# Kernel tuning notes

Measured on AMD Instinct MI355X. Metric: run time of the kernel, lower is better.

## Reference

```python
import jax, jax.numpy as jnp
import numpy as np

U, I, H, E, EL = 100000, 50000, 128, 600000, 200000


def setup_inputs() -> dict:
    key = jax.random.key(0)
    ks = jax.random.split(key, 24)
    inp = {}
    inp["user_emb"] = jax.random.normal(ks[0], (U, H), jnp.float32) * 0.1
    inp["item_emb"] = jax.random.normal(ks[1], (I, H), jnp.float32) * 0.1
    s = 1.0 / np.sqrt(H)
    names = ["w1_ui_l", "w1_ui_r", "w1_iu_l", "w1_iu_r",
             "w2_ui_l", "w2_ui_r", "w2_iu_l", "w2_iu_r"]
    for i, n in enumerate(names):
        inp[n] = jax.random.uniform(ks[2 + i], (H, H), jnp.float32, -s, s)
    for i, n in enumerate(["b1_ui", "b1_iu", "b2_ui", "b2_iu"]):
        inp[n] = jax.random.uniform(ks[10 + i], (H,), jnp.float32, -s, s)
    inp["user_node_id"] = jnp.arange(U, dtype=jnp.int32)
    inp["item_node_id"] = jnp.arange(I, dtype=jnp.int32)
    src_u = jax.random.randint(ks[14], (E,), 0, U, jnp.int32)
    dst_i = jax.random.randint(ks[15], (E,), 0, I, jnp.int32)
    inp["edge_index_ui"] = jnp.stack([src_u, dst_i])  # user -> item
    inp["edge_index_iu"] = jnp.stack([dst_i, src_u])  # item -> user (reverse)
    lu = jax.random.randint(ks[16], (EL,), 0, U, jnp.int32)
    li = jax.random.randint(ks[17], (EL,), 0, I, jnp.int32)
    inp["edge_label_index"] = jnp.stack([lu, li])
    return inp


def _sage(x_src, x_dst, edge_index, w_l, b_l, w_r, num_dst):
    # PyG SAGEConv: out = lin_l(mean_j x_src[j]) + lin_r(x_dst)
    src, dst = edge_index[0], edge_index[1]
    msg = x_src[src]                                   # [E, H] gather
    agg = jax.ops.segment_sum(msg, dst, num_segments=num_dst)
    cnt = jax.ops.segment_sum(jnp.ones((msg.shape[0],), msg.dtype), dst,
                              num_segments=num_dst)
    mean = agg / jnp.maximum(cnt, 1.0)[:, None]
    return mean @ w_l + b_l + x_dst @ w_r


def reference(user_emb, item_emb,
              w1_ui_l, w1_ui_r, w1_iu_l, w1_iu_r,
              w2_ui_l, w2_ui_r, w2_iu_l, w2_iu_r,
              b1_ui, b1_iu, b2_ui, b2_iu,
              user_node_id, item_node_id,
              edge_index_ui, edge_index_iu, edge_label_index):
    xu = user_emb[user_node_id]   # [U, H]
    xi = item_emb[item_node_id]   # [I, H]
    # layer 1 (hetero: each dst type aggregates from its single incoming relation)
    u1 = jax.nn.relu(_sage(xi, xu, edge_index_iu, w1_iu_l, b1_iu, w1_iu_r, U))
    i1 = jax.nn.relu(_sage(xu, xi, edge_index_ui, w1_ui_l, b1_ui, w1_ui_r, I))
    # layer 2
    u2 = _sage(i1, u1, edge_index_iu, w2_iu_l, b2_iu, w2_iu_r, U)
    i2 = _sage(u1, i1, edge_index_ui, w2_ui_l, b2_ui, w2_ui_r, I)
    # edge-indexed dot-product classifier
    fu = u2[edge_label_index[0]]  # [EL, H]
    fi = i2[edge_label_index[1]]  # [EL, H]
    return jnp.sum(fu * fi, axis=-1)
```

## Files before the change

### kernel.cpp

```cpp
#include <hip/hip_runtime.h>
#include <hip/hip_bf16.h>
#include <cstdio>

#define U_N 100000
#define I_N 50000
#define H_DIM 128
#define E_N 600000
#define EL_N 200000

#define EPB 2048
#define NBLK ((E_N + EPB - 1) / EPB)
#define SH_U 8
#define SH_I 7
#define NB_U ((U_N + 255) >> 8)
#define NB_I ((I_N + 127) >> 7)
#define LH_U (NB_U * NBLK)
#define LH_I (NB_I * NBLK)
#define LH_TOT (LH_U + LH_I)

#define CVT_BLK (((U_N + I_N) * 16) / 256)
#define PREP_BLK 512
#define NBU2 ((U_N + 255) / 256)
#define NBI2 ((I_N + 255) / 256)

typedef __attribute__((ext_vector_type(8))) short bh8;
typedef __attribute__((ext_vector_type(4))) float f32x4;
typedef __attribute__((ext_vector_type(8))) unsigned short u16x8;

__device__ inline unsigned short f2b(float f) {
  unsigned u = __builtin_bit_cast(unsigned, f);
  u += 0x7fffu + ((u >> 16) & 1u);
  return (unsigned short)(u >> 16);
}
__device__ inline float b2f(unsigned short h) {
  unsigned u = ((unsigned)h) << 16;
  return __builtin_bit_cast(float, u);
}

__global__ __launch_bounds__(256) void prep_all(
    const float* __restrict__ xu, const float* __restrict__ xi,
    const int* __restrict__ unid, const int* __restrict__ inid,
    unsigned short* __restrict__ ub, unsigned short* __restrict__ ib,
    const float* __restrict__ l0, const float* __restrict__ r0, short* __restrict__ o0,
    const float* __restrict__ l1, const float* __restrict__ r1, short* __restrict__ o1,
    const float* __restrict__ l2, const float* __restrict__ r2, short* __restrict__ o2,
    const float* __restrict__ l3, const float* __restrict__ r3, short* __restrict__ o3,
    const int* __restrict__ e_ui, int* __restrict__ hist) {
  __shared__ int h[512];
  const int b = blockIdx.x;
  const int tid = threadIdx.x;
  if (b < CVT_BLK) {
    int t = b * 256 + tid;
    const float* x;
    unsigned short* xb;
    int row, seg;
    if (t < U_N * 16) {
      row = t >> 4; seg = t & 15;
      int r0_ = row;
      row = unid ? unid[row] : row;
      x = xu; xb = ub + (size_t)r0_ * H_DIM;
    } else {
      int t2 = t - U_N * 16;
      row = t2 >> 4; seg = t2 & 15;
      int r0_ = row;
      row = inid ? inid[row] : row;
      x = xi; xb = ib + (size_t)r0_ * H_DIM;
    }
    const float* p = x + (size_t)row * H_DIM + seg * 8;
    float4 a = ((const float4*)p)[0];
    float4 c = ((const float4*)p)[1];
    u16x8 v;
    v[0] = f2b(a.x); v[1] = f2b(a.y); v[2] = f2b(a.z); v[3] = f2b(a.w);
    v[4] = f2b(c.x); v[5] = f2b(c.y); v[6] = f2b(c.z); v[7] = f2b(c.w);
    *(u16x8*)(xb + seg * 8) = v;
  } else if (b < CVT_BLK + PREP_BLK) {
    int t = (b - CVT_BLK) * 256 + tid;
    int set = t >> 15, s = t & 32767;
    const float *wl, *wr; short* W2;
    if (set == 0)      { wl = l0; wr = r0; W2 = o0; }
    else if (set == 1) { wl = l1; wr = r1; W2 = o1; }
    else if (set == 2) { wl = l2; wr = r2; W2 = o2; }
    else               { wl = l3; wr = r3; W2 = o3; }
    int col = s >> 8, k = s & 255;
    float v = (k < 128) ? wl[k * 128 + col] : wr[(k - 128) * 128 + col];
    W2[col * 256 + k] = (short)f2b(v);
  } else {
    int hb = b - CVT_BLK - PREP_BLK;
    int side = hb >= NBLK;
    int blk = side ? hb - NBLK : hb;
    const int* dst = e_ui + (side ? E_N : 0);
    int shift = side ? SH_I : SH_U;
    int nbins = side ? NB_I : NB_U;
    int hbase = side ? LH_U : 0;
    for (int i = tid; i < nbins; i += 256) h[i] = 0;
    __syncthreads();
    const int base = blk * EPB;
    const int end = min(base + EPB, E_N);
    for (int i = base + tid; i < end; i += 256)
      atomicAdd(&h[((unsigned)dst[i]) >> shift], 1);
    __syncthreads();
    for (int i = tid; i < nbins; i += 256)
      hist[hbase + i * NBLK + blk] = h[i];
  }
}

__global__ __launch_bounds__(256) void scan_p1(const int* __restrict__ cnt,
                                               int* __restrict__ bsum, int n) {
  const int t = threadIdx.x;
  const int base = blockIdx.x * 1024 + t * 4;
  int s = 0;
  for (int j = 0; j < 4; ++j) {
    int i = base + j;
    if (i < n) s += cnt[i];
  }
  for (int off = 32; off > 0; off >>= 1) s += __shfl_down(s, off, 64);
  __shared__ int wsum[4];
  if ((t & 63) == 0) wsum[t >> 6] = s;
  __syncthreads();
  if (t == 0) bsum[blockIdx.x] = wsum[0] + wsum[1] + wsum[2] + wsum[3];
}

__global__ __launch_bounds__(256) void scan_p2(int* __restrict__ bsum, int nb) {
  __shared__ int sm[256];
  const int t = threadIdx.x;
  int v = (t < nb) ? bsum[t] : 0;
  sm[t] = v;
  __syncthreads();
  for (int d = 1; d < 256; d <<= 1) {
    int x = (t >= d) ? sm[t - d] : 0;
    __syncthreads();
    sm[t] += x;
    __syncthreads();
  }
  if (t < nb) bsum[t] = sm[t] - v;
}

__global__ __launch_bounds__(256) void scan_p3(const int* __restrict__ cnt,
                                               const int* __restrict__ bsum,
                                               int* __restrict__ off, int n) {
  const int t = threadIdx.x;
  const int lane = t & 63, wv = t >> 6;
  const int base = blockIdx.x * 1024 + t * 4;
  int vals[4];
  int s = 0;
  for (int j = 0; j < 4; ++j) {
    int i = base + j;
    vals[j] = (i < n) ? cnt[i] : 0;
    s += vals[j];
  }
  int inc = s;
  for (int d = 1; d < 64; d <<= 1) {
    int x = __shfl_up(inc, d, 64);
    if (lane >= d) inc += x;
  }
  __shared__ int wsum[4];
  if (lane == 63) wsum[wv] = inc;
  __syncthreads();
  int wbase = 0;
  for (int w = 0; w < wv; ++w) wbase += wsum[w];
  int excl = wbase + (inc - s) + bsum[blockIdx.x];
  for (int j = 0; j < 4; ++j) {
    int i = base + j;
    if (i < n) off[i] = excl;
    excl += vals[j];
  }
}

__global__ __launch_bounds__(256) void bin_scatter2(const int* __restrict__ e_ui,
                                                    const int* __restrict__ hoff,
                                                    unsigned* __restrict__ bucketed) {
  __shared__ int cur[512];
  const int t = threadIdx.x;
  const int hb = blockIdx.x;
  const int side = hb >= NBLK;
  const int blk = side ? hb - NBLK : hb;
  const int* dst = e_ui + (side ? E_N : 0);
  const int* src = e_ui + (side ? 0 : E_N);
  const int shift = side ? SH_I : SH_U;
  const int nbins = side ? NB_I : NB_U;
  const int hbase = side ? LH_U : 0;
  for (int i = t; i < nbins; i += 256) cur[i] = hoff[hbase + i * NBLK + blk];
  __syncthreads();
  const int base = blk * EPB;
  const int end = min(base + EPB, E_N);
  const unsigned mask = (1u << shift) - 1u;
  for (int i = base + t; i < end; i += 256) {
    unsigned d = (unsigned)dst[i];
    int bin = (int)(d >> shift);
    int pos = atomicAdd(&cur[bin], 1);
    bucketed[pos] = ((d & mask) << 24) | (unsigned)src[i];
  }
}

__global__ __launch_bounds__(256) void bin_group2(const int* __restrict__ hoff,
                                                  const unsigned* __restrict__ bucketed,
                                                  int* __restrict__ csr,
                                                  int* __restrict__ cnt_u,
                                                  int* __restrict__ off_u,
                                                  int* __restrict__ cnt_i,
                                                  int* __restrict__ off_i) {
  __shared__ int cl[256];
  __shared__ int cur[256];
  __shared__ int wsum[4];
  const int b = blockIdx.x;
  const int t = threadIdx.x;
  const int side = b >= NB_U;
  const int bb = side ? b - NB_U : b;
  const int shift = side ? SH_I : SH_U;
  const int N = side ? I_N : U_N;
  int* cnt = side ? cnt_i : cnt_u;
  int* off = side ? off_i : off_u;
  int start, end;
  if (!side) {
    start = hoff[bb * NBLK];
    end = (bb + 1 < NB_U) ? hoff[(bb + 1) * NBLK] : E_N;
  } else {
    start = hoff[LH_U + bb * NBLK];
    end = (bb + 1 < NB_I) ? hoff[LH_U + (bb + 1) * NBLK] : 2 * E_N;
  }
  const int ndst = 1 << shift;
  const int base = bb << shift;
  if (t < ndst) cl[t] = 0;
  __syncthreads();
  for (int i = start + t; i < end; i += 256)
    atomicAdd(&cl[bucketed[i] >> 24], 1);
  __syncthreads();
  int v = (t < ndst) ? cl[t] : 0;
  const int lane = t & 63, wv = t >> 6;
  int inc = v;
  for (int d = 1; d < 64; d <<= 1) {
    int x = __shfl_up(inc, d, 64);
    if (lane >= d) inc += x;
  }
  if (lane == 63) wsum[wv] = inc;
  __syncthreads();
  int wbase = 0;
  for (int q = 0; q < wv; ++q) wbase += wsum[q];
  int excl = wbase + inc - v;
  if (t < ndst) {
    cur[t] = start + excl;
    int node = base + t;
    if (node < N) { cnt[node] = v; off[node] = start + excl; }
  }
  __syncthreads();
  for (int i = start + t; i < end; i += 256) {
    unsigned w = bucketed[i];
    int pos = atomicAdd(&cur[w >> 24], 1);
    csr[pos] = (int)(w & 0xFFFFFFu);
  }
}

__global__ __launch_bounds__(256) void gather_mean2(
    const int* __restrict__ off_u, const int* __restrict__ cnt_u,
    const unsigned short* __restrict__ xsrc_u, unsigned short* __restrict__ agg_u,
    const int* __restrict__ off_i, const int* __restrict__ cnt_i,
    const unsigned short* __restrict__ xsrc_i, unsigned short* __restrict__ agg_i,
    const int* __restrict__ csr) {
  long t = (long)blockIdx.x * 256 + threadIdx.x;
  int node = (int)(t >> 4);
  int lane = (int)(t & 15);
  const int* off; const int* cnt;
  const unsigned short* xb; unsigned short* aggb;
  if (node < U_N) {
    off = off_u; cnt = cnt_u; xb = xsrc_u; aggb = agg_u;
  } else {
    node -= U_N;
    if (node >= I_N) return;
    off = off_i; cnt = cnt_i; xb = xsrc_i; aggb = agg_i;
  }
  int o = off[node], c = cnt[node];
  float acc[8] = {};
  for (int j0 = 0; j0 < c; j0 += 16) {
    int nj = c - j0;
    if (nj > 16) nj = 16;
    int sidx = (lane < nj) ? csr[o + j0 + lane] : 0;
    int j = 0;
    for (; j + 8 <= nj; j += 8) {
      u16x8 v[8];
      for (int m = 0; m < 8; ++m) {
        int s = __shfl(sidx, j + m, 16);
        v[m] = *(const u16x8*)(xb + (size_t)s * H_DIM + lane * 8);
      }
      for (int m = 0; m < 8; ++m)
        for (int k = 0; k < 8; ++k) acc[k] += b2f(v[m][k]);
    }
    for (; j + 4 <= nj; j += 4) {
      u16x8 v[4];
      for (int m = 0; m < 4; ++m) {
        int s = __shfl(sidx, j + m, 16);
        v[m] = *(const u16x8*)(xb + (size_t)s * H_DIM + lane * 8);
      }
      for (int m = 0; m < 4; ++m)
        for (int k = 0; k < 8; ++k) acc[k] += b2f(v[m][k]);
    }
    for (; j < nj; ++j) {
      int s = __shfl(sidx, j, 16);
      u16x8 v = *(const u16x8*)(xb + (size_t)s * H_DIM + lane * 8);
      for (int k = 0; k < 8; ++k) acc[k] += b2f(v[k]);
    }
  }
  float inv = 1.0f / (float)(c > 0 ? c : 1);
  u16x8 r;
  for (int k = 0; k < 8; ++k) r[k] = f2b(acc[k] * inv);
  *(u16x8*)(aggb + (size_t)node * H_DIM + lane * 8) = r;
}

__global__ __launch_bounds__(256, 2) void sage_gemm2(
    const unsigned short* __restrict__ agg_u, const unsigned short* __restrict__ x_u,
    const short* __restrict__ W2_u, const float* __restrict__ bias_u,
    unsigned short* __restrict__ out_u,
    const unsigned short* __restrict__ agg_i, const unsigned short* __restrict__ x_i,
    const short* __restrict__ W2_i, const float* __restrict__ bias_i,
    unsigned short* __restrict__ out_i, int relu) {
  const unsigned short *aggb, *xb;
  const short* W2;
  const float* bias;
  unsigned short* outb;
  int N, blk;
  if (blockIdx.x < NBU2) {
    aggb = agg_u; xb = x_u; W2 = W2_u; bias = bias_u; outb = out_u;
    N = U_N; blk = blockIdx.x;
  } else {
    aggb = agg_i; xb = x_i; W2 = W2_i; bias = bias_i; outb = out_i;
    N = I_N; blk = blockIdx.x - NBU2;
  }

  __shared__ short wlds[128 * 256];
  const int tid = threadIdx.x;
  for (int c = tid; c < 4096; c += 256) {
    int col = c >> 5, g = c & 31;
    uint4 v = *(const uint4*)(W2 + col * 256 + g * 8);
    *(uint4*)(&wlds[col * 256 + ((g ^ (col & 15)) * 8)]) = v;
  }
  __syncthreads();

  const int lane = tid & 63;
  const int wave = tid >> 6;
  const int q = lane >> 4;
  const int n16 = lane & 15;
  const int rowbase = blk * 256 + wave * 64;

  const unsigned short* aptr[4];
  const unsigned short* xptr[4];
  for (int g = 0; g < 4; ++g) {
    int row = rowbase + g * 16 + n16;
    int rr = row < N ? row : 0;
    aptr[g] = aggb + (size_t)rr * H_DIM + q * 8;
    xptr[g] = xb + (size_t)rr * H_DIM + q * 8;
  }

  f32x4 acc[4][8] = {};

  for (int kt = 0; kt < 8; ++kt) {
    const int k0 = kt * 32;
    bh8 afrag[4];
    for (int g = 0; g < 4; ++g) {
      const unsigned short* p = (kt < 4) ? (aptr[g] + k0) : (xptr[g] + (k0 - 128));
      afrag[g] = *(const bh8*)(p);
    }
    const int swz = ((kt * 4 + q) ^ n16) * 8;
    for (int c = 0; c < 8; ++c) {
      bh8 b = *(const bh8*)(&wlds[(c * 16 + n16) * 256 + swz]);
      acc[0][c] = __builtin_amdgcn_mfma_f32_16x16x32_bf16(afrag[0], b, acc[0][c], 0, 0, 0);
      acc[1][c] = __builtin_amdgcn_mfma_f32_16x16x32_bf16(afrag[1], b, acc[1][c], 0, 0, 0);
      acc[2][c] = __builtin_amdgcn_mfma_f32_16x16x32_bf16(afrag[2], b, acc[2][c], 0, 0, 0);
      acc[3][c] = __builtin_amdgcn_mfma_f32_16x16x32_bf16(afrag[3], b, acc[3][c], 0, 0, 0);
    }
  }

  float bcol[8];
  for (int c = 0; c < 8; ++c) bcol[c] = bias[c * 16 + n16];

  for (int g = 0; g < 4; ++g) {
    for (int r = 0; r < 4; ++r) {
      int row = rowbase + g * 16 + q * 4 + r;
      if (row >= N) continue;
      for (int c = 0; c < 8; ++c) {
        float v = acc[g][c][r] + bcol[c];
        if (relu) v = v > 0.0f ? v : 0.0f;
        outb[(size_t)row * H_DIM + c * 16 + n16] = f2b(v);
      }
    }
  }
}

__global__ __launch_bounds__(256) void final_dot(const int* __restrict__ lbl,
                                                 const unsigned short* __restrict__ u2,
                                                 const unsigned short* __restrict__ i2,
                                                 float* __restrict__ out) {
  long t = (long)blockIdx.x * 256 + threadIdx.x;
  int e = (int)(t >> 4);
  if (e >= EL_N) return;
  int lane = (int)(t & 15);
  int lu = lbl[e];
  int li = lbl[EL_N + e];
  u16x8 a = *(const u16x8*)(u2 + (size_t)lu * H_DIM + lane * 8);
  u16x8 b = *(const u16x8*)(i2 + (size_t)li * H_DIM + lane * 8);
  float p = 0.f;
  for (int k = 0; k < 8; ++k) p += b2f(a[k]) * b2f(b[k]);
  for (int off = 8; off > 0; off >>= 1) p += __shfl_down(p, off, 16);
  if (lane == 0) out[e] = p;
}

extern "C" void kernel_launch(void* const* d_in, const int* in_sizes, int n_in,
                              void* d_out, int out_size, void* d_ws, size_t ws_size,
                              hipStream_t stream) {
  const float* user_emb = (const float*)d_in[0];
  const float* item_emb = (const float*)d_in[1];
  const float* w1_ui_l = (const float*)d_in[2];
  const float* w1_ui_r = (const float*)d_in[3];
  const float* w1_iu_l = (const float*)d_in[4];
  const float* w1_iu_r = (const float*)d_in[5];
  const float* w2_ui_l = (const float*)d_in[6];
  const float* w2_ui_r = (const float*)d_in[7];
  const float* w2_iu_l = (const float*)d_in[8];
  const float* w2_iu_r = (const float*)d_in[9];
  const float* b1_ui = (const float*)d_in[10];
  const float* b1_iu = (const float*)d_in[11];
  const float* b2_ui = (const float*)d_in[12];
  const float* b2_iu = (const float*)d_in[13];
  const int* unid = (const int*)d_in[14];
  const int* inid = (const int*)d_in[15];
  const int* e_ui = (const int*)d_in[16];
  const int* e_iu = (const int*)d_in[17];
  const int* elbl = (const int*)d_in[18];
  float* out = (float*)d_out;

  char* ws = (char*)d_ws;
  size_t o = 0;
  auto alloc = [&](size_t bytes) {
    char* p = ws + o;
    o = (o + bytes + 255) & ~(size_t)255;
    return p;
  };
  int* hist = (int*)alloc((size_t)LH_TOT * 4);
  int* hoff = (int*)alloc((size_t)LH_TOT * 4);
  unsigned* bkt = (unsigned*)alloc((size_t)2 * E_N * 4);
  int* csr = (int*)alloc((size_t)2 * E_N * 4);
  int* cnt_u = (int*)alloc((size_t)U_N * 4);
  int* cnt_i = (int*)alloc((size_t)I_N * 4);
  int* off_u = (int*)alloc((size_t)U_N * 4);
  int* off_i = (int*)alloc((size_t)I_N * 4);
  int* bsum = (int*)alloc(256 * 4);
  unsigned short* ue_b = (unsigned short*)alloc((size_t)U_N * H_DIM * 2);
  unsigned short* ie_b = (unsigned short*)alloc((size_t)I_N * H_DIM * 2);
  unsigned short* agg_u = (unsigned short*)alloc((size_t)U_N * H_DIM * 2);
  unsigned short* agg_i = (unsigned short*)alloc((size_t)I_N * H_DIM * 2);
  unsigned short* h1_u = (unsigned short*)alloc((size_t)U_N * H_DIM * 2);
  unsigned short* h1_i = (unsigned short*)alloc((size_t)I_N * H_DIM * 2);
  unsigned short* h2_u = (unsigned short*)alloc((size_t)U_N * H_DIM * 2);
  unsigned short* h2_i = (unsigned short*)alloc((size_t)I_N * H_DIM * 2);
  short* W2_1u = (short*)alloc(128 * 256 * 2);
  short* W2_1i = (short*)alloc(128 * 256 * 2);
  short* W2_2u = (short*)alloc(128 * 256 * 2);
  short* W2_2i = (short*)alloc(128 * 256 * 2);
  if (o > ws_size) {
    fprintf(stderr, "kernel_launch: ws too small, need %zu have %zu\n", o, ws_size);
    return;
  }

  prep_all<<<CVT_BLK + PREP_BLK + 2 * NBLK, 256, 0, stream>>>(
      user_emb, item_emb, unid, inid, ue_b, ie_b,
      w1_iu_l, w1_iu_r, W2_1u, w1_ui_l, w1_ui_r, W2_1i,
      w2_iu_l, w2_iu_r, W2_2u, w2_ui_l, w2_ui_r, W2_2i,
      e_ui, hist);

  const int nb1 = (LH_TOT + 1023) / 1024;
  scan_p1<<<nb1, 256, 0, stream>>>(hist, bsum, LH_TOT);
  scan_p2<<<1, 256, 0, stream>>>(bsum, nb1);
  scan_p3<<<nb1, 256, 0, stream>>>(hist, bsum, hoff, LH_TOT);

  bin_scatter2<<<2 * NBLK, 256, 0, stream>>>(e_ui, hoff, bkt);
  bin_group2<<<NB_U + NB_I, 256, 0, stream>>>(hoff, bkt, csr, cnt_u, off_u, cnt_i, off_i);

  const int g_blocks = ((U_N + I_N) * 16 + 255) / 256;
  gather_mean2<<<g_blocks, 256, 0, stream>>>(off_u, cnt_u, ie_b, agg_u,
                                             off_i, cnt_i, ue_b, agg_i, csr);
  sage_gemm2<<<NBU2 + NBI2, 256, 0, stream>>>(
      agg_u, ue_b, W2_1u, b1_iu, h1_u,
      agg_i, ie_b, W2_1i, b1_ui, h1_i, 1);

  gather_mean2<<<g_blocks, 256, 0, stream>>>(off_u, cnt_u, h1_i, agg_u,
                                             off_i, cnt_i, h1_u, agg_i, csr);
  sage_gemm2<<<NBU2 + NBI2, 256, 0, stream>>>(
      agg_u, h1_u, W2_2u, b2_iu, h2_u,
      agg_i, h1_i, W2_2i, b2_ui, h2_i, 0);

  final_dot<<<(EL_N * 16 + 255) / 256, 256, 0, stream>>>(elbl, h2_u, h2_i, out);
}
```

Measured before the change: 361.9 us.

## Fuse neighbor mean aggregation with SAGE GEMM in one kernel

Replaces the separate gather-mean and GEMM kernels with a single fused kernel per layer. Each block of 128 destination nodes computes the neighbor means into LDS, loads its self features into swizzled LDS, and runs MFMA against weights held in registers, with each wave covering 32 output columns. This drops the global write and re-read of the aggregation buffers and two launches. The trade-off is that the gather phase now sits inside a GEMM block with 64KB of LDS and heavy register use, which may lower occupancy and the latency hiding available to the irregular gathers.

```diff
diff --git a/kernel.cpp b/kernel.cpp
--- a/kernel.cpp
+++ b/kernel.cpp
@@ -20,8 +20,8 @@
 
 #define CVT_BLK (((U_N + I_N) * 16) / 256)
 #define PREP_BLK 512
-#define NBU2 ((U_N + 255) / 256)
-#define NBI2 ((I_N + 255) / 256)
+#define NBU3 ((U_N + 127) / 128)
+#define NBI3 ((I_N + 127) / 128)
 
 typedef __attribute__((ext_vector_type(8))) short bh8;
 typedef __attribute__((ext_vector_type(4))) float f32x4;
@@ -250,135 +250,111 @@
   }
 }
 
-__global__ __launch_bounds__(256) void gather_mean2(
+__global__ __launch_bounds__(256, 2) void sage_fused(
     const int* __restrict__ off_u, const int* __restrict__ cnt_u,
-    const unsigned short* __restrict__ xsrc_u, unsigned short* __restrict__ agg_u,
-    const int* __restrict__ off_i, const int* __restrict__ cnt_i,
-    const unsigned short* __restrict__ xsrc_i, unsigned short* __restrict__ agg_i,
-    const int* __restrict__ csr) {
-  long t = (long)blockIdx.x * 256 + threadIdx.x;
-  int node = (int)(t >> 4);
-  int lane = (int)(t & 15);
-  const int* off; const int* cnt;
-  const unsigned short* xb; unsigned short* aggb;
-  if (node < U_N) {
-    off = off_u; cnt = cnt_u; xb = xsrc_u; aggb = agg_u;
-  } else {
-    node -= U_N;
-    if (node >= I_N) return;
-    off = off_i; cnt = cnt_i; xb = xsrc_i; aggb = agg_i;
-  }
-  int o = off[node], c = cnt[node];
-  float acc[8] = {};
-  for (int j0 = 0; j0 < c; j0 += 16) {
-    int nj = c - j0;
-    if (nj > 16) nj = 16;
-    int sidx = (lane < nj) ? csr[o + j0 + lane] : 0;
-    int j = 0;
-    for (; j + 8 <= nj; j += 8) {
-      u16x8 v[8];
-      for (int m = 0; m < 8; ++m) {
-        int s = __shfl(sidx, j + m, 16);
-        v[m] = *(const u16x8*)(xb + (size_t)s * H_DIM + lane * 8);
-      }
-      for (int m = 0; m < 8; ++m)
-        for (int k = 0; k < 8; ++k) acc[k] += b2f(v[m][k]);
-    }
-    for (; j + 4 <= nj; j += 4) {
-      u16x8 v[4];
-      for (int m = 0; m < 4; ++m) {
-        int s = __shfl(sidx, j + m, 16);
-        v[m] = *(const u16x8*)(xb + (size_t)s * H_DIM + lane * 8);
-      }
-      for (int m = 0; m < 4; ++m)
-        for (int k = 0; k < 8; ++k) acc[k] += b2f(v[m][k]);
-    }
-    for (; j < nj; ++j) {
-      int s = __shfl(sidx, j, 16);
-      u16x8 v = *(const u16x8*)(xb + (size_t)s * H_DIM + lane * 8);
-      for (int k = 0; k < 8; ++k) acc[k] += b2f(v[k]);
-    }
-  }
-  float inv = 1.0f / (float)(c > 0 ? c : 1);
-  u16x8 r;
-  for (int k = 0; k < 8; ++k) r[k] = f2b(acc[k] * inv);
-  *(u16x8*)(aggb + (size_t)node * H_DIM + lane * 8) = r;
-}
-
-__global__ __launch_bounds__(256, 2) void sage_gemm2(
-    const unsigned short* __restrict__ agg_u, const unsigned short* __restrict__ x_u,
+    const unsigned short* __restrict__ src_u,
+    const unsigned short* __restrict__ x_u,
     const short* __restrict__ W2_u, const float* __restrict__ bias_u,
     unsigned short* __restrict__ out_u,
-    const unsigned short* __restrict__ agg_i, const unsigned short* __restrict__ x_i,
+    const int* __restrict__ off_i, const int* __restrict__ cnt_i,
+    const unsigned short* __restrict__ src_i,
+    const unsigned short* __restrict__ x_i,
     const short* __restrict__ W2_i, const float* __restrict__ bias_i,
-    unsigned short* __restrict__ out_i, int relu) {
-  const unsigned short *aggb, *xb;
-  const short* W2;
-  const float* bias;
-  unsigned short* outb;
+    unsigned short* __restrict__ out_i,
+    const int* __restrict__ csr, int relu) {
+  __shared__ unsigned short mlds[128 * 128];
+  __shared__ unsigned short xlds[128 * 128];
+  const int* off; const int* cnt;
+  const unsigned short *srcx, *xself;
+  const short* W2; const float* bias; unsigned short* outb;
   int N, blk;
-  if (blockIdx.x < NBU2) {
-    aggb = agg_u; xb = x_u; W2 = W2_u; bias = bias_u; outb = out_u;
-    N = U_N; blk = blockIdx.x;
+  if (blockIdx.x < NBU3) {
+    off = off_u; cnt = cnt_u; srcx = src_u; xself = x_u;
+    W2 = W2_u; bias = bias_u; outb = out_u; N = U_N; blk = blockIdx.x;
   } else {
-    aggb = agg_i; xb = x_i; W2 = W2_i; bias = bias_i; outb = out_i;
-    N = I_N; blk = blockIdx.x - NBU2;
-  }
-
-  __shared__ short wlds[128 * 256];
+    off = off_i; cnt = cnt_i; srcx = src_i; xself = x_i;
+    W2 = W2_i; bias = bias_i; outb = out_i; N = I_N; blk = blockIdx.x - NBU3;
+  }
+  const int rowbase = blk * 128;
   const int tid = threadIdx.x;
-  for (int c = tid; c < 4096; c += 256) {
-    int col = c >> 5, g = c & 31;
-    uint4 v = *(const uint4*)(W2 + col * 256 + g * 8);
-    *(uint4*)(&wlds[col * 256 + ((g ^ (col & 15)) * 8)]) = v;
-  }
-  __syncthreads();
-
-  const int lane = tid & 63;
-  const int wave = tid >> 6;
-  const int q = lane >> 4;
-  const int n16 = lane & 15;
-  const int rowbase = blk * 256 + wave * 64;
-
-  const unsigned short* aptr[4];
-  const unsigned short* xptr[4];
-  for (int g = 0; g < 4; ++g) {
-    int row = rowbase + g * 16 + n16;
-    int rr = row < N ? row : 0;
-    aptr[g] = aggb + (size_t)rr * H_DIM + q * 8;
-    xptr[g] = xb + (size_t)rr * H_DIM + q * 8;
-  }
-
-  f32x4 acc[4][8] = {};
-
-  for (int kt = 0; kt < 8; ++kt) {
-    const int k0 = kt * 32;
-    bh8 afrag[4];
-    for (int g = 0; g < 4; ++g) {
-      const unsigned short* p = (kt < 4) ? (aptr[g] + k0) : (xptr[g] + (k0 - 128));
-      afrag[g] = *(const bh8*)(p);
+  const int lane = tid & 63, wave = tid >> 6;
+  const int n16 = lane & 15, q = lane >> 4;
+
+  bh8 bfrag[8][2];
+  for (int kt = 0; kt < 8; ++kt)
+    for (int j = 0; j < 2; ++j)
+      bfrag[kt][j] = *(const bh8*)(W2 + ((wave * 2 + j) * 16 + n16) * 256 + kt * 32 + q * 8);
+
+  for (int it = 0; it < 8; ++it) {
+    int idx = it * 256 + tid;
+    int local = idx >> 4, g = idx & 15;
+    int rr = rowbase + local;
+    if (rr >= N) rr = N - 1;
+    u16x8 v = *(const u16x8*)(xself + (size_t)rr * H_DIM + g * 8);
+    *(u16x8*)(&xlds[local * H_DIM + ((g ^ (local & 15)) * 8)]) = v;
+  }
+
+  const int gid = tid >> 4, l16 = tid & 15;
+  for (int it = 0; it < 8; ++it) {
+    int local = it * 16 + gid;
+    int node = rowbase + local;
+    float acc[8] = {};
+    int c = 0;
+    if (node < N) {
+      int o = off[node];
+      c = cnt[node];
+      for (int j0 = 0; j0 < c; j0 += 16) {
+        int nj = c - j0;
+        if (nj > 16) nj = 16;
+        int sidx = (l16 < nj) ? csr[o + j0 + l16] : 0;
+        int j = 0;
+        for (; j + 4 <= nj; j += 4) {
+          u16x8 v[4];
+          for (int m = 0; m < 4; ++m) {
+            int s = __shfl(sidx, j + m, 16);
+            v[m] = *(const u16x8*)(srcx + (size_t)s * H_DIM + l16 * 8);
+          }
+          for (int m = 0; m < 4; ++m)
+            for (int k = 0; k < 8; ++k) acc[k] += b2f(v[m][k]);
+        }
+        for (; j < nj; ++j) {
+          int s = __shfl(sidx, j, 16);
+          u16x8 v = *(const u16x8*)(srcx + (size_t)s * H_DIM + l16 * 8);
+          for (int k = 0; k < 8; ++k) acc[k] += b2f(v[k]);
+        }
+      }
     }
-    const int swz = ((kt * 4 + q) ^ n16) * 8;
-    for (int c = 0; c < 8; ++c) {
-      bh8 b = *(const bh8*)(&wlds[(c * 16 + n16) * 256 + swz]);
-      acc[0][c] = __builtin_amdgcn_mfma_f32_16x16x32_bf16(afrag[0], b, acc[0][c], 0, 0, 0);
-      acc[1][c] = __builtin_amdgcn_mfma_f32_16x16x32_bf16(afrag[1], b, acc[1][c], 0, 0, 0);
-      acc[2][c] = __builtin_amdgcn_mfma_f32_16x16x32_bf16(afrag[2], b, acc[2][c], 0, 0, 0);
-      acc[3][c] = __builtin_amdgcn_mfma_f32_16x16x32_bf16(afrag[3], b, acc[3][c], 0, 0, 0);
+    float inv = 1.0f / (float)(c > 0 ? c : 1);
+    u16x8 r;
+    for (int k = 0; k < 8; ++k) r[k] = f2b(acc[k] * inv);
+    *(u16x8*)(&mlds[local * H_DIM + ((l16 ^ (local & 15)) * 8)]) = r;
+  }
+  __syncthreads();
+
+  f32x4 acc[8][2] = {};
+  for (int g = 0; g < 8; ++g) {
+    const int lr = g * 16 + n16;
+    for (int kt = 0; kt < 8; ++kt) {
+      const int G = (kt & 3) * 4 + q;
+      const unsigned short* base_ = (kt < 4) ? mlds : xlds;
+      bh8 a = *(const bh8*)(base_ + lr * H_DIM + ((G ^ n16) * 8));
+      acc[g][0] = __builtin_amdgcn_mfma_f32_16x16x32_bf16(a, bfrag[kt][0], acc[g][0], 0, 0, 0);
+      acc[g][1] = __builtin_amdgcn_mfma_f32_16x16x32_bf16(a, bfrag[kt][1], acc[g][1], 0, 0, 0);
     }
   }
 
-  float bcol[8];
-  for (int c = 0; c < 8; ++c) bcol[c] = bias[c * 16 + n16];
-
-  for (int g = 0; g < 4; ++g) {
+  float bc[2];
+  bc[0] = bias[(wave * 2 + 0) * 16 + n16];
+  bc[1] = bias[(wave * 2 + 1) * 16 + n16];
+
+  for (int g = 0; g < 8; ++g) {
     for (int r = 0; r < 4; ++r) {
       int row = rowbase + g * 16 + q * 4 + r;
       if (row >= N) continue;
-      for (int c = 0; c < 8; ++c) {
-        float v = acc[g][c][r] + bcol[c];
+      for (int j = 0; j < 2; ++j) {
+        float v = acc[g][j][r] + bc[j];
         if (relu) v = v > 0.0f ? v : 0.0f;
-        outb[(size_t)row * H_DIM + c * 16 + n16] = f2b(v);
+        outb[(size_t)row * H_DIM + (wave * 2 + j) * 16 + n16] = f2b(v);
       }
     }
   }
@@ -444,8 +420,6 @@
   int* bsum = (int*)alloc(256 * 4);
   unsigned short* ue_b = (unsigned short*)alloc((size_t)U_N * H_DIM * 2);
   unsigned short* ie_b = (unsigned short*)alloc((size_t)I_N * H_DIM * 2);
-  unsigned short* agg_u = (unsigned short*)alloc((size_t)U_N * H_DIM * 2);
-  unsigned short* agg_i = (unsigned short*)alloc((size_t)I_N * H_DIM * 2);
   unsigned short* h1_u = (unsigned short*)alloc((size_t)U_N * H_DIM * 2);
   unsigned short* h1_i = (unsigned short*)alloc((size_t)I_N * H_DIM * 2);
   unsigned short* h2_u = (unsigned short*)alloc((size_t)U_N * H_DIM * 2);
@@ -473,18 +447,15 @@
   bin_scatter2<<<2 * NBLK, 256, 0, stream>>>(e_ui, hoff, bkt);
   bin_group2<<<NB_U + NB_I, 256, 0, stream>>>(hoff, bkt, csr, cnt_u, off_u, cnt_i, off_i);
 
-  const int g_blocks = ((U_N + I_N) * 16 + 255) / 256;
-  gather_mean2<<<g_blocks, 256, 0, stream>>>(off_u, cnt_u, ie_b, agg_u,
-                                             off_i, cnt_i, ue_b, agg_i, csr);
-  sage_gemm2<<<NBU2 + NBI2, 256, 0, stream>>>(
-      agg_u, ue_b, W2_1u, b1_iu, h1_u,
-      agg_i, ie_b, W2_1i, b1_ui, h1_i, 1);
-
-  gather_mean2<<<g_blocks, 256, 0, stream>>>(off_u, cnt_u, h1_i, agg_u,
-                                             off_i, cnt_i, h1_u, agg_i, csr);
-  sage_gemm2<<<NBU2 + NBI2, 256, 0, stream>>>(
-      agg_u, h1_u, W2_2u, b2_iu, h2_u,
-      agg_i, h1_i, W2_2i, b2_ui, h2_i, 0);
+  sage_fused<<<NBU3 + NBI3, 256, 0, stream>>>(
+      off_u, cnt_u, ie_b, ue_b, W2_1u, b1_iu, h1_u,
+      off_i, cnt_i, ue_b, ie_b, W2_1i, b1_ui, h1_i,
+      csr, 1);
+
+  sage_fused<<<NBU3 + NBI3, 256, 0, stream>>>(
+      off_u, cnt_u, h1_i, h1_u, W2_2u, b2_iu, h2_u,
+      off_i, cnt_i, h1_u, h1_i, W2_2i, b2_ui, h2_i,
+      csr, 0);
 
   final_dot<<<(EL_N * 16 + 255) / 256, 256, 0, stream>>>(elbl, h2_u, h2_i, out);
 }
```

Measured after the change: 431.0 us. 19.1% more time.
